# Performance work log

Measured on AMD Instinct MI355X. Metric: run time of the kernel, lower is better.

Reference implementation:

```python
import jax, jax.numpy as jnp
import numpy as np

B, N, FEAT, H, E, L = 4096, 64, 32, 128, 4, 3  # batch, node_num, node feat, hidden_dim, edge_dim, hidden_num


def setup_inputs() -> dict:
    key = jax.random.key(0)
    ks = jax.random.split(key, 12)
    s = 0.05
    x = jax.random.normal(ks[0], (B, N, FEAT), dtype=jnp.float32)
    adj = jax.random.uniform(ks[1], (B, E, N, N), dtype=jnp.float32)
    # per-node input/output embeddings (stacked over node index)
    in_w = jax.random.normal(ks[2], (N, FEAT, H), dtype=jnp.float32) * s
    in_b = jax.random.normal(ks[3], (N, H), dtype=jnp.float32) * s
    out_w = jax.random.normal(ks[4], (N, H, FEAT), dtype=jnp.float32) * s
    out_b = jax.random.normal(ks[5], (N, FEAT), dtype=jnp.float32) * s
    # relational GC weights per layer: (L, E, H, H) and bias (L, E, 1, H)
    gc_w = jax.random.normal(ks[6], (L, E, H, H), dtype=jnp.float32) * s
    gc_b = jax.random.normal(ks[7], (L, E, 1, H), dtype=jnp.float32) * s
    # GRU params, gate order [r, z, n] like torch
    w_ih = jax.random.normal(ks[8], (3 * H, H), dtype=jnp.float32) * s
    w_hh = jax.random.normal(ks[9], (3 * H, H), dtype=jnp.float32) * s
    b_ih = jax.random.normal(ks[10], (3 * H,), dtype=jnp.float32) * s
    b_hh = jax.random.normal(ks[11], (3 * H,), dtype=jnp.float32) * s
    return {"x": x, "adj": adj, "in_w": in_w, "in_b": in_b, "out_w": out_w,
            "out_b": out_b, "gc_w": gc_w, "gc_b": gc_b, "w_ih": w_ih,
            "w_hh": w_hh, "b_ih": b_ih, "b_hh": b_hh}


def _gru_step(xf, h, w_ih, w_hh, b_ih, b_hh):
    # xf, h: (B*N, H); single-timestep torch GRU cell
    gi = xf @ w_ih.T + b_ih
    gh = h @ w_hh.T + b_hh
    i_r, i_z, i_n = jnp.split(gi, 3, axis=-1)
    h_r, h_z, h_n = jnp.split(gh, 3, axis=-1)
    r = jax.nn.sigmoid(i_r + h_r)
    z = jax.nn.sigmoid(i_z + h_z)
    n = jnp.tanh(i_n + r * h_n)
    return (1.0 - z) * n + z * h


def reference(x, adj, in_w, in_b, out_w, out_b, gc_w, gc_b, w_ih, w_hh, b_ih, b_hh):
    # per-node input embedding: (B, N, FEAT) -> (B, N, H)
    h = jnp.einsum('bnd,ndh->bnh', x, in_w) + in_b
    hidden = h.reshape(-1, H)  # initial GRU hidden = embedded input
    cur = h
    for i in range(L):
        # relational GCN: per-edge-type projection + adjacency matmul + bias + relu + mean over edge types
        support = jnp.einsum('bid,edh->beih', cur, gc_w[i])
        out = jnp.einsum('beij,bejh->beih', adj, support) + gc_b[i]
        out = jax.nn.relu(out)
        agg = jnp.mean(out, axis=1)  # (B, N, H)
        hidden = _gru_step(agg.reshape(-1, H), hidden, w_ih, w_hh, b_ih, b_hh)
        cur = hidden.reshape(B, N, H)
    # per-node output embedding, zero-padded back to hidden width
    feats = jnp.einsum('bnh,nhd->bnd', cur, out_w) + out_b  # (B, N, FEAT)
    return jnp.pad(feats, ((0, 0), (0, 0), (0, H - FEAT)))
```

## Files before the change

### kernel.cpp

```cpp
#include <hip/hip_runtime.h>
#include <cstdint>

#define NBATCH 4096
#define NNODE  64
#define FEAT   32
#define H      128
#define NE     4
#define NL     3

typedef __attribute__((ext_vector_type(8))) short short8;
typedef __attribute__((ext_vector_type(4))) short short4v;
typedef __attribute__((ext_vector_type(4))) float f32x4;
typedef __attribute__((ext_vector_type(2))) float f32x2;
typedef unsigned long long u64;
typedef unsigned short ushort;

#define IMG_GC_ELEMS   (128 * 64)
#define IMG_GRU_ELEMS  (48 * 128)
#define IMG_GC_BYTES   (24 * IMG_GC_ELEMS * 2)
#define IMG_GRU_BYTES  (16 * IMG_GRU_ELEMS * 2)
#define WS_W_BYTES     (IMG_GC_BYTES + IMG_GRU_BYTES)
#define WIMG_SHORTS    (WS_W_BYTES / 2)
#define ADJ_IMG_ELEMS  4096
#define WS_FULL ((size_t)WS_W_BYTES + (size_t)NBATCH * NE * ADJ_IMG_ELEMS * 2)

__device__ __forceinline__ ushort f2b(float f) {
  union { float f; unsigned u; } v; v.f = f;
  unsigned u = v.u + 0x7FFFu + ((v.u >> 16) & 1u);
  return (ushort)(u >> 16);
}
__device__ __forceinline__ float b2f(ushort s) {
  union { unsigned u; float f; } v; v.u = ((unsigned)s) << 16;
  return v.f;
}
__device__ __forceinline__ unsigned cvtpk(float lo, float hi) {
  unsigned r;
  asm volatile("v_cvt_pk_bf16_f32 %0, %1, %2" : "=v"(r) : "v"(lo), "v"(hi));
  return r;
}
__device__ __forceinline__ u64 pk4(float a, float b, float c, float d) {
  return (u64)cvtpk(a, b) | ((u64)cvtpk(c, d) << 32);
}
__device__ __forceinline__ float sigm(float v) { return 1.0f / (1.0f + __expf(-v)); }
__device__ __forceinline__ float tanh_(float v) {
  v = fminf(fmaxf(v, -15.f), 15.f);
  float e = __expf(-2.f * v);
  return (1.f - e) / (1.f + e);
}
__device__ __forceinline__ int gidx128(int r, int g) { return r * 128 + ((g ^ (r & 7)) << 3); }
__device__ __forceinline__ int idx128(int r, int k) { return gidx128(r, k >> 3) + (k & 7); }
__device__ __forceinline__ int gidx64(int r, int g) { return r * 64 + (((g ^ (r & 7)) & 7) << 3); }

__device__ __forceinline__ short8 pack8f(const float* v) {
  union { unsigned u[4]; short8 s; } r;
  r.u[0] = cvtpk(v[0], v[1]); r.u[1] = cvtpk(v[2], v[3]);
  r.u[2] = cvtpk(v[4], v[5]); r.u[3] = cvtpk(v[6], v[7]);
  return r.s;
}

__device__ __forceinline__ void gll16(const void* g, void* l) {
  __builtin_amdgcn_global_load_lds(
      (const __attribute__((address_space(1))) unsigned int*)g,
      (__attribute__((address_space(3))) unsigned int*)l, 16, 0, 0);
}

#define STAGE(dst, src, NIT)                                             \
  do {                                                                   \
    _Pragma("unroll")                                                    \
    for (int it_ = 0; it_ < (NIT); ++it_) {                              \
      int off_ = (it_ * 4 + w) * 1024;                                   \
      gll16((const char*)(src) + off_ + lane * 16, (char*)(dst) + off_); \
    }                                                                    \
  } while (0)

#define BAR() do { asm volatile("s_waitcnt lgkmcnt(0)" ::: "memory"); \
                   __builtin_amdgcn_s_barrier(); } while (0)
#define VMW(N) do { asm volatile("s_waitcnt vmcnt(" #N ")" ::: "memory"); \
                    __builtin_amdgcn_sched_barrier(0); } while (0)
#define SB0() __builtin_amdgcn_sched_barrier(0)

__global__ __launch_bounds__(256, 2) void k_prep(
    const float* __restrict__ gc_w, const float* __restrict__ w_ih,
    const float* __restrict__ w_hh, ushort* __restrict__ ws)
{
  const int t = threadIdx.x;
  if (blockIdx.x < 24) {
    const int blk = blockIdx.x;
    const int kh = blk & 1, e = (blk >> 1) & 3, l = blk >> 3;
    const float* We = gc_w + (size_t)(l * NE + e) * H * H;
    ushort* dst = ws + (size_t)blk * IMG_GC_ELEMS;
    #pragma unroll
    for (int it = 0; it < 4; ++it) {
      int idx = t + it * 256;
      int r = idx >> 3, g = idx & 7;
      float v[8];
      #pragma unroll
      for (int j = 0; j < 8; ++j) v[j] = We[(kh * 64 + g * 8 + j) * H + r];
      *(short8*)&dst[gidx64(r, g)] = pack8f(v);
    }
  } else {
    const int blk = blockIdx.x - 24;
    const int c = blk & 7, m = blk >> 3;
    const float* Mat = m ? w_hh : w_ih;
    ushort* dst = ws + WIMG_SHORTS - IMG_GRU_BYTES / 2 + (size_t)blk * IMG_GRU_ELEMS;
    #pragma unroll
    for (int it = 0; it < 3; ++it) {
      int idx = t + it * 256;
      int rr = idx >> 4, g = idx & 15;
      int mrow = (rr >> 4) * H + 16 * c + (rr & 15);
      float v[8];
      #pragma unroll
      for (int j = 0; j < 8; ++j) v[j] = Mat[mrow * H + g * 8 + j];
      *(short8*)&dst[gidx128(rr, g)] = pack8f(v);
    }
  }
}

template <bool ADJIMG>
__global__ __launch_bounds__(256, 2) void k_inemb(
    const float* __restrict__ x, const float* __restrict__ in_w,
    const float* __restrict__ in_b, const float* __restrict__ adj,
    ushort* __restrict__ ws, float* __restrict__ out)
{
  __shared__ float s_wt[FEAT * H];
  __shared__ float s_x[64 * FEAT];
  const int t = threadIdx.x;
  const int n = blockIdx.x >> 6, bt = blockIdx.x & 63, b0 = bt * 64;
  const float* wsrc = in_w + (size_t)n * FEAT * H;
  #pragma unroll
  for (int it = 0; it < 4; ++it) {
    int i4 = t + it * 256;
    *(f32x4*)&s_wt[i4 * 4] = *(const f32x4*)&wsrc[i4 * 4];
  }
  {
    int r = t >> 2, q = t & 3;
    const float* xs = x + ((size_t)(b0 + r) * NNODE + n) * FEAT;
    *(f32x4*)&s_x[r * 32 + q * 8]     = *(const f32x4*)&xs[q * 8];
    *(f32x4*)&s_x[r * 32 + q * 8 + 4] = *(const f32x4*)&xs[q * 8 + 4];
  }
  __syncthreads();
  const int h2 = t & 63, rp = t >> 6;
  const float bi0 = in_b[n * H + 2 * h2], bi1 = in_b[n * H + 2 * h2 + 1];
  #pragma unroll 1
  for (int m = 0; m < 16; ++m) {
    int r = rp + 4 * m;
    float a0 = bi0, a1 = bi1;
    #pragma unroll
    for (int d = 0; d < 32; ++d) {
      float xv = s_x[r * 32 + d];
      f32x2 wv = *(const f32x2*)&s_wt[d * H + 2 * h2];
      a0 += xv * wv.x; a1 += xv * wv.y;
    }
    unsigned p = cvtpk(a0, a1);
    ushort* tail = (ushort*)(out + ((size_t)(b0 + r) * NNODE + n) * H + 64);
    *(unsigned*)(tail + 2 * h2) = p;
  }
  if (ADJIMG) {
    const float* ab = adj + (size_t)blockIdx.x * NE * NNODE * NNODE;
    ushort* dst = ws + WIMG_SHORTS + (size_t)blockIdx.x * NE * ADJ_IMG_ELEMS;
    #pragma unroll 1
    for (int q = 0; q < 8; ++q) {
      int gi = t + q * 256;
      int e = gi >> 9, idx = gi & 511, r = idx >> 3, g = idx & 7;
      const float* src = ab + e * 4096 + r * 64 + g * 8;
      float v[8];
      #pragma unroll
      for (int j = 0; j < 8; ++j) v[j] = src[j];
      *(short8*)&dst[e * ADJ_IMG_ELEMS + gidx64(r, g)] = pack8f(v);
    }
  }
}

template <bool ADJIMG>
__global__ __launch_bounds__(256, 2) void k_main(
    const float* __restrict__ adj,
    const float* __restrict__ gc_b,
    const float* __restrict__ b_ih, const float* __restrict__ b_hh,
    const ushort* __restrict__ wimg,
    float* __restrict__ out)
{
  __shared__ ushort s_u[128 * 64];
  __shared__ ushort s_stage[24576];
  __shared__ float s_bias[1280];

  ushort* w0    = s_stage;
  ushort* w1    = s_stage + 8192;
  ushort* sadj  = s_stage + 16384;
  ushort* gru0  = s_stage;
  ushort* gru1  = s_stage + 12288;

  const int t = threadIdx.x;
  const int b = blockIdx.x;
  const int w = t >> 6, lane = t & 63, lr = lane & 15, lq = lane >> 4;
  const int wm = w & 1, wn = w >> 1;
  float* outb = out + (size_t)b * NNODE * H;
  const ushort* img_gru = wimg + WIMG_SHORTS - IMG_GRU_BYTES / 2;
  const ushort* aimg = wimg + WIMG_SHORTS + (size_t)b * NE * ADJ_IMG_ELEMS;

  STAGE(w0, wimg, 4);
  short8 cur[2][4];
  #pragma unroll
  for (int rt = 0; rt < 2; ++rt)
    #pragma unroll
    for (int ks = 0; ks < 4; ++ks) {
      int node = 32 * wm + 16 * rt + lr;
      cur[rt][ks] = *(const short8*)((const ushort*)(outb + (size_t)node * H + 64) + 32 * ks + 8 * lq);
    }
  #pragma unroll
  for (int it = 0; it < 3; ++it) {
    int idx = t + it * 256;
    s_bias[512 + idx] = (idx < 384) ? b_ih[idx] : b_hh[idx - 384];
  }
  __syncthreads();

  #pragma unroll 1
  for (int layer = 0; layer < NL; ++layer) {
    f32x4 agg[2][4];
    #pragma unroll
    for (int mt = 0; mt < 2; ++mt)
      #pragma unroll
      for (int nt = 0; nt < 4; ++nt) agg[mt][nt] = f32x4{0.f, 0.f, 0.f, 0.f};

    #pragma unroll 1
    for (int e = 0; e < NE; ++e) {
      const ushort* img_e = wimg + (size_t)((layer * NE + e) * 2) * IMG_GC_ELEMS;

      if (e == 0) {
        s_bias[t]       = gc_b[layer * 512 + t];
        s_bias[t + 256] = gc_b[layer * 512 + t + 256];
      }
      STAGE(w1, img_e + IMG_GC_ELEMS, 4);
      SB0();
      if (ADJIMG) {
        STAGE(sadj, aimg + (size_t)e * ADJ_IMG_ELEMS, 2);
        SB0();
      } else {
        const float* adj_e = adj + (((size_t)b * NE + e) * NNODE * NNODE);
        #pragma unroll
        for (int it = 0; it < 2; ++it) {
          int idx = t + it * 256;
          int i = idx >> 3, g = idx & 7;
          const float* src = adj_e + i * 64 + g * 8;
          float v[8];
          #pragma unroll
          for (int j = 0; j < 8; ++j) v[j] = src[j];
          *(short8*)&sadj[gidx64(i, g)] = pack8f(v);
        }
      }
      f32x4 Sacc[2][4];
      #pragma unroll
      for (int mt = 0; mt < 2; ++mt)
        #pragma unroll
        for (int nt = 0; nt < 4; ++nt) Sacc[mt][nt] = f32x4{0.f, 0.f, 0.f, 0.f};
      if (ADJIMG) VMW(6);
      __builtin_amdgcn_s_setprio(1);
      #pragma unroll
      for (int ks = 0; ks < 2; ++ks) {
        #pragma unroll
        for (int nt = 0; nt < 4; ++nt) {
          short8 bb = *(const short8*)&w0[gidx64(64 * wn + 16 * nt + lr, ks * 4 + lq)];
          #pragma unroll
          for (int mt = 0; mt < 2; ++mt)
            Sacc[mt][nt] = __builtin_amdgcn_mfma_f32_16x16x32_bf16(cur[mt][ks], bb, Sacc[mt][nt], 0, 0, 0);
        }
      }
      __builtin_amdgcn_s_setprio(0);
      if (ADJIMG) { VMW(2); BAR(); } else __syncthreads();

      if (e < 3) { STAGE(w0, img_e + 2 * IMG_GC_ELEMS, 4); }
      else       { STAGE(gru0, img_gru, 3); }
      SB0();
      __builtin_amdgcn_s_setprio(1);
      #pragma unroll
      for (int ks = 0; ks < 2; ++ks) {
        #pragma unroll
        for (int nt = 0; nt < 4; ++nt) {
          short8 bb = *(const short8*)&w1[gidx64(64 * wn + 16 * nt + lr, ks * 4 + lq)];
          #pragma unroll
          for (int mt = 0; mt < 2; ++mt)
            Sacc[mt][nt] = __builtin_amdgcn_mfma_f32_16x16x32_bf16(cur[mt][2 + ks], bb, Sacc[mt][nt], 0, 0, 0);
        }
      }
      __builtin_amdgcn_s_setprio(0);
      #pragma unroll
      for (int mt = 0; mt < 2; ++mt) {
        int j0 = 32 * wm + 16 * mt + 4 * lq;
        #pragma unroll
        for (int nt = 0; nt < 4; ++nt) {
          int h = 64 * wn + 16 * nt + lr;
          *(u64*)&s_u[gidx64(h, j0 >> 3) + (j0 & 7)] =
              pk4(Sacc[mt][nt][0], Sacc[mt][nt][1], Sacc[mt][nt][2], Sacc[mt][nt][3]);
        }
      }
      if (ADJIMG) { if (e < 3) { VMW(4); } else { VMW(3); } BAR(); } else __syncthreads();

      if (e == 3) { STAGE(gru0 + 6144, img_gru + IMG_GRU_ELEMS, 3); SB0(); }
      {
        f32x4 Oacc[2][4];
        #pragma unroll
        for (int mt = 0; mt < 2; ++mt)
          #pragma unroll
          for (int nt = 0; nt < 4; ++nt) Oacc[mt][nt] = f32x4{0.f, 0.f, 0.f, 0.f};
        __builtin_amdgcn_s_setprio(1);
        #pragma unroll
        for (int ks = 0; ks < 2; ++ks) {
          short8 a[2];
          #pragma unroll
          for (int mt = 0; mt < 2; ++mt)
            a[mt] = *(const short8*)&sadj[gidx64(32 * wm + 16 * mt + lr, ks * 4 + lq)];
          #pragma unroll
          for (int nt = 0; nt < 4; ++nt) {
            short8 bb = *(const short8*)&s_u[gidx64(64 * wn + 16 * nt + lr, ks * 4 + lq)];
            #pragma unroll
            for (int mt = 0; mt < 2; ++mt)
              Oacc[mt][nt] = __builtin_amdgcn_mfma_f32_16x16x32_bf16(a[mt], bb, Oacc[mt][nt], 0, 0, 0);
          }
        }
        __builtin_amdgcn_s_setprio(0);
        #pragma unroll
        for (int mt = 0; mt < 2; ++mt)
          #pragma unroll
          for (int nt = 0; nt < 4; ++nt) {
            float bias = s_bias[e * 128 + 64 * wn + 16 * nt + lr];
            #pragma unroll
            for (int r = 0; r < 4; ++r)
              agg[mt][nt][r] += 0.25f * fmaxf(Oacc[mt][nt][r] + bias, 0.f);
          }
      }
      if (ADJIMG) { BAR(); } else __syncthreads();
    }

    #pragma unroll
    for (int mt = 0; mt < 2; ++mt)
      #pragma unroll
      for (int nt = 0; nt < 4; ++nt) {
        int h = 64 * wn + 16 * nt + lr;
        #pragma unroll
        for (int r = 0; r < 4; ++r)
          s_u[idx128(32 * wm + 16 * mt + 4 * lq + r, h)] = f2b(agg[mt][nt][r]);
      }
    __syncthreads();

    #pragma unroll 1
    for (int p = 0; p < 4; ++p) {
      const int cc = 2 * p + wn;
      const ushort* ihb = gru0 + wn * 6144;
      const ushort* hhb = gru1 + wn * 6144;
      STAGE(gru1, img_gru + (size_t)(8 + 2 * p) * IMG_GRU_ELEMS, 3);
      STAGE(gru1 + 6144, img_gru + (size_t)(8 + 2 * p + 1) * IMG_GRU_ELEMS, 3);
      SB0();
      short4v holdv[2];
      #pragma unroll
      for (int nst = 0; nst < 2; ++nst) {
        int node = 16 * (2 * wm + nst) + lr;
        holdv[nst] = *(const short4v*)((const ushort*)(outb + (size_t)node * H + 64) + 16 * cc + 4 * lq);
      }
      f32x4 gi[3][2];
      #pragma unroll
      for (int tg = 0; tg < 3; ++tg)
        #pragma unroll
        for (int nst = 0; nst < 2; ++nst) gi[tg][nst] = f32x4{0.f, 0.f, 0.f, 0.f};
      __builtin_amdgcn_s_setprio(1);
      #pragma unroll
      for (int ks = 0; ks < 4; ++ks) {
        short8 bb[2];
        #pragma unroll
        for (int nst = 0; nst < 2; ++nst)
          bb[nst] = *(const short8*)&s_u[gidx128(16 * (2 * wm + nst) + lr, ks * 4 + lq)];
        #pragma unroll
        for (int tg = 0; tg < 3; ++tg) {
          short8 a = *(const short8*)&ihb[gidx128(16 * tg + lr, ks * 4 + lq)];
          #pragma unroll
          for (int nst = 0; nst < 2; ++nst)
            gi[tg][nst] = __builtin_amdgcn_mfma_f32_16x16x32_bf16(a, bb[nst], gi[tg][nst], 0, 0, 0);
        }
      }
      __builtin_amdgcn_s_setprio(0);
      __syncthreads();

      if (p < 3) {
        STAGE(gru0, img_gru + (size_t)(2 * (p + 1)) * IMG_GRU_ELEMS, 3);
        STAGE(gru0 + 6144, img_gru + (size_t)(2 * (p + 1) + 1) * IMG_GRU_ELEMS, 3);
      } else if (layer < 2) {
        STAGE(w0, wimg + (size_t)((layer + 1) * NE * 2) * IMG_GC_ELEMS, 4);
      }
      SB0();
      f32x4 gh[3][2];
      #pragma unroll
      for (int tg = 0; tg < 3; ++tg)
        #pragma unroll
        for (int nst = 0; nst < 2; ++nst) gh[tg][nst] = f32x4{0.f, 0.f, 0.f, 0.f};
      __builtin_amdgcn_s_setprio(1);
      #pragma unroll
      for (int ks = 0; ks < 4; ++ks) {
        #pragma unroll
        for (int tg = 0; tg < 3; ++tg) {
          short8 a = *(const short8*)&hhb[gidx128(16 * tg + lr, ks * 4 + lq)];
          #pragma unroll
          for (int nst = 0; nst < 2; ++nst)
            gh[tg][nst] = __builtin_amdgcn_mfma_f32_16x16x32_bf16(a, cur[nst][ks], gh[tg][nst], 0, 0, 0);
        }
      }
      __builtin_amdgcn_s_setprio(0);
      #pragma unroll
      for (int nst = 0; nst < 2; ++nst) {
        int node = 16 * (2 * wm + nst) + lr;
        float hf[4];
        #pragma unroll
        for (int r = 0; r < 4; ++r) {
          int mH = 16 * cc + 4 * lq + r;
          float rg = sigm(gi[0][nst][r] + s_bias[512 + mH] + gh[0][nst][r] + s_bias[896 + mH]);
          float zg = sigm(gi[1][nst][r] + s_bias[640 + mH] + gh[1][nst][r] + s_bias[1024 + mH]);
          float ng = tanh_(gi[2][nst][r] + s_bias[768 + mH] + rg * (gh[2][nst][r] + s_bias[1152 + mH]));
          float hold = b2f((ushort)holdv[nst][r]);
          hf[r] = (1.f - zg) * ng + zg * hold;
        }
        *(u64*)((ushort*)(outb + (size_t)node * H + 64) + 16 * cc + 4 * lq) =
            pk4(hf[0], hf[1], hf[2], hf[3]);
      }
      __syncthreads();
    }

    if (layer < 2) {
      #pragma unroll
      for (int rt = 0; rt < 2; ++rt)
        #pragma unroll
        for (int ks = 0; ks < 4; ++ks) {
          int node = 32 * wm + 16 * rt + lr;
          cur[rt][ks] = *(const short8*)((const ushort*)(outb + (size_t)node * H + 64) + 32 * ks + 8 * lq);
        }
    }
  }
}

__global__ __launch_bounds__(256, 2) void k_outemb(
    const float* __restrict__ out_w, const float* __restrict__ out_b,
    float* __restrict__ out)
{
  __shared__ float s_wt[H * FEAT];
  __shared__ float s_c[64 * 132];
  const int t = threadIdx.x;
  const int n = blockIdx.x >> 6, bt = blockIdx.x & 63, b0 = bt * 64;
  const float* wsrc = out_w + (size_t)n * H * FEAT;
  #pragma unroll
  for (int it = 0; it < 4; ++it) {
    int i4 = t + it * 256;
    *(f32x4*)&s_wt[i4 * 4] = *(const f32x4*)&wsrc[i4 * 4];
  }
  #pragma unroll
  for (int it = 0; it < 4; ++it) {
    int idx = t + it * 256;
    int r = idx >> 4, g = idx & 15;
    const ushort* tail = (const ushort*)(out + ((size_t)(b0 + r) * NNODE + n) * H + 64);
    short8 v = *(const short8*)(tail + g * 8);
    #pragma unroll
    for (int j = 0; j < 8; ++j) s_c[r * 132 + g * 8 + j] = b2f((ushort)v[j]);
  }
  __syncthreads();
  const int d = t & 31, rq = t >> 5;
  const float bias = out_b[n * FEAT + d];
  float accs[8];
  #pragma unroll
  for (int m = 0; m < 8; ++m) {
    int r = rq + 8 * m;
    float a = bias;
    #pragma unroll 8
    for (int k = 0; k < H; ++k) a += s_c[r * 132 + k] * s_wt[k * FEAT + d];
    accs[m] = a;
  }
  #pragma unroll
  for (int m = 0; m < 8; ++m) {
    int r = rq + 8 * m;
    out[((size_t)(b0 + r) * NNODE + n) * H + d] = accs[m];
  }
  #pragma unroll
  for (int q = 0; q < 6; ++q) {
    int idx = t + q * 256;
    int r = idx / 24, c4 = idx - r * 24;
    *(f32x4*)&out[((size_t)(b0 + r) * NNODE + n) * H + FEAT + c4 * 4] =
        f32x4{0.f, 0.f, 0.f, 0.f};
  }
}

extern "C" void kernel_launch(void* const* d_in, const int* in_sizes, int n_in,
                              void* d_out, int out_size, void* d_ws, size_t ws_size,
                              hipStream_t stream) {
  const float* x     = (const float*)d_in[0];
  const float* adj   = (const float*)d_in[1];
  const float* in_w  = (const float*)d_in[2];
  const float* in_b  = (const float*)d_in[3];
  const float* out_w = (const float*)d_in[4];
  const float* out_b = (const float*)d_in[5];
  const float* gc_w  = (const float*)d_in[6];
  const float* gc_b  = (const float*)d_in[7];
  const float* w_ih  = (const float*)d_in[8];
  const float* w_hh  = (const float*)d_in[9];
  const float* b_ih  = (const float*)d_in[10];
  const float* b_hh  = (const float*)d_in[11];
  (void)in_sizes; (void)n_in; (void)out_size;
  ushort* wimg = (ushort*)d_ws;
  const bool full = ws_size >= WS_FULL;
  hipLaunchKernelGGL(k_prep, dim3(40), dim3(256), 0, stream, gc_w, w_ih, w_hh, wimg);
  if (full) {
    hipLaunchKernelGGL(k_inemb<true>, dim3(NBATCH), dim3(256), 0, stream,
                       x, in_w, in_b, adj, wimg, (float*)d_out);
    hipLaunchKernelGGL(k_main<true>, dim3(NBATCH), dim3(256), 0, stream,
                       adj, gc_b, b_ih, b_hh, wimg, (float*)d_out);
  } else {
    hipLaunchKernelGGL(k_inemb<false>, dim3(NBATCH), dim3(256), 0, stream,
                       x, in_w, in_b, adj, wimg, (float*)d_out);
    hipLaunchKernelGGL(k_main<false>, dim3(NBATCH), dim3(256), 0, stream,
                       adj, gc_b, b_ih, b_hh, wimg, (float*)d_out);
  }
  hipLaunchKernelGGL(k_outemb, dim3(NBATCH), dim3(256), 0, stream, out_w, out_b, (float*)d_out);
}
```

Baseline: 763.9 us.

## Read weight fragments directly from global memory instead of staging through LDS

Removes the double-buffered LDS staging (global_load_lds, waitcnt and sched barriers) for the GC and GRU weight images. The MFMA B/A fragments are now loaded straight from global memory and served by the L2/L1 caches. This shrinks shared memory enough to raise launch bounds to 4 blocks per CU and drops several barriers. In exchange, every wave issues redundant global loads with exposed latency and loses the explicit prefetch overlap.

```diff
diff --git a/kernel.cpp b/kernel.cpp
--- a/kernel.cpp
+++ b/kernel.cpp
@@ -73,11 +73,8 @@
     }                                                                    \
   } while (0)
 
-#define BAR() do { asm volatile("s_waitcnt lgkmcnt(0)" ::: "memory"); \
-                   __builtin_amdgcn_s_barrier(); } while (0)
-#define VMW(N) do { asm volatile("s_waitcnt vmcnt(" #N ")" ::: "memory"); \
-                    __builtin_amdgcn_sched_barrier(0); } while (0)
-#define SB0() __builtin_amdgcn_sched_barrier(0)
+#define MFMA16(A, B, C) __builtin_amdgcn_mfma_f32_16x16x32_bf16((A), (B), (C), 0, 0, 0)
+#define GFRAG(base, off) (*(const short8*)&(base)[(off)])
 
 __global__ __launch_bounds__(256, 2) void k_prep(
     const float* __restrict__ gc_w, const float* __restrict__ w_ih,
@@ -172,40 +169,30 @@
 }
 
 template <bool ADJIMG>
-__global__ __launch_bounds__(256, 2) void k_main(
+__global__ __launch_bounds__(256, 4) void k_main(
     const float* __restrict__ adj,
     const float* __restrict__ gc_b,
     const float* __restrict__ b_ih, const float* __restrict__ b_hh,
     const ushort* __restrict__ wimg,
     float* __restrict__ out)
 {
-  __shared__ ushort s_u[128 * 64];
-  __shared__ ushort s_stage[24576];
-  __shared__ float s_bias[1280];
-
-  ushort* w0    = s_stage;
-  ushort* w1    = s_stage + 8192;
-  ushort* sadj  = s_stage + 16384;
-  ushort* gru0  = s_stage;
-  ushort* gru1  = s_stage + 12288;
-
-  const int t = threadIdx.x;
-  const int b = blockIdx.x;
+  __shared__ ushort s_u[8192];
+  __shared__ ushort s_adj[4096];
+  __shared__ float  s_bias[1280];
+
+  const int t = threadIdx.x, b = blockIdx.x;
   const int w = t >> 6, lane = t & 63, lr = lane & 15, lq = lane >> 4;
   const int wm = w & 1, wn = w >> 1;
   float* outb = out + (size_t)b * NNODE * H;
   const ushort* img_gru = wimg + WIMG_SHORTS - IMG_GRU_BYTES / 2;
   const ushort* aimg = wimg + WIMG_SHORTS + (size_t)b * NE * ADJ_IMG_ELEMS;
 
-  STAGE(w0, wimg, 4);
   short8 cur[2][4];
   #pragma unroll
-  for (int rt = 0; rt < 2; ++rt)
-    #pragma unroll
-    for (int ks = 0; ks < 4; ++ks) {
-      int node = 32 * wm + 16 * rt + lr;
-      cur[rt][ks] = *(const short8*)((const ushort*)(outb + (size_t)node * H + 64) + 32 * ks + 8 * lq);
-    }
+  for (int mt = 0; mt < 2; ++mt)
+    #pragma unroll
+    for (int ks = 0; ks < 4; ++ks)
+      cur[mt][ks] = *(const short8*)((const ushort*)(outb + (size_t)(32 * wm + 16 * mt + lr) * H + 64) + 32 * ks + 8 * lq);
   #pragma unroll
   for (int it = 0; it < 3; ++it) {
     int idx = t + it * 256;
@@ -224,16 +211,12 @@
     #pragma unroll 1
     for (int e = 0; e < NE; ++e) {
       const ushort* img_e = wimg + (size_t)((layer * NE + e) * 2) * IMG_GC_ELEMS;
-
       if (e == 0) {
         s_bias[t]       = gc_b[layer * 512 + t];
         s_bias[t + 256] = gc_b[layer * 512 + t + 256];
       }
-      STAGE(w1, img_e + IMG_GC_ELEMS, 4);
-      SB0();
       if (ADJIMG) {
-        STAGE(sadj, aimg + (size_t)e * ADJ_IMG_ELEMS, 2);
-        SB0();
+        STAGE(s_adj, aimg + (size_t)e * ADJ_IMG_ELEMS, 2);
       } else {
         const float* adj_e = adj + (((size_t)b * NE + e) * NNODE * NNODE);
         #pragma unroll
@@ -244,7 +227,7 @@
           float v[8];
           #pragma unroll
           for (int j = 0; j < 8; ++j) v[j] = src[j];
-          *(short8*)&sadj[gidx64(i, g)] = pack8f(v);
+          *(short8*)&s_adj[gidx64(i, g)] = pack8f(v);
         }
       }
       f32x4 Sacc[2][4];
@@ -252,33 +235,19 @@
       for (int mt = 0; mt < 2; ++mt)
         #pragma unroll
         for (int nt = 0; nt < 4; ++nt) Sacc[mt][nt] = f32x4{0.f, 0.f, 0.f, 0.f};
-      if (ADJIMG) VMW(6);
       __builtin_amdgcn_s_setprio(1);
       #pragma unroll
-      for (int ks = 0; ks < 2; ++ks) {
-        #pragma unroll
-        for (int nt = 0; nt < 4; ++nt) {
-          short8 bb = *(const short8*)&w0[gidx64(64 * wn + 16 * nt + lr, ks * 4 + lq)];
-          #pragma unroll
-          for (int mt = 0; mt < 2; ++mt)
-            Sacc[mt][nt] = __builtin_amdgcn_mfma_f32_16x16x32_bf16(cur[mt][ks], bb, Sacc[mt][nt], 0, 0, 0);
-        }
-      }
-      __builtin_amdgcn_s_setprio(0);
-      if (ADJIMG) { VMW(2); BAR(); } else __syncthreads();
-
-      if (e < 3) { STAGE(w0, img_e + 2 * IMG_GC_ELEMS, 4); }
-      else       { STAGE(gru0, img_gru, 3); }
-      SB0();
-      __builtin_amdgcn_s_setprio(1);
-      #pragma unroll
-      for (int ks = 0; ks < 2; ++ks) {
-        #pragma unroll
-        for (int nt = 0; nt < 4; ++nt) {
-          short8 bb = *(const short8*)&w1[gidx64(64 * wn + 16 * nt + lr, ks * 4 + lq)];
-          #pragma unroll
-          for (int mt = 0; mt < 2; ++mt)
-            Sacc[mt][nt] = __builtin_amdgcn_mfma_f32_16x16x32_bf16(cur[mt][2 + ks], bb, Sacc[mt][nt], 0, 0, 0);
+      for (int kh = 0; kh < 2; ++kh) {
+        const ushort* wb = img_e + (size_t)kh * IMG_GC_ELEMS;
+        #pragma unroll
+        for (int ks = 0; ks < 2; ++ks) {
+          #pragma unroll
+          for (int nt = 0; nt < 4; ++nt) {
+            short8 bb = GFRAG(wb, gidx64(64 * wn + 16 * nt + lr, ks * 4 + lq));
+            #pragma unroll
+            for (int mt = 0; mt < 2; ++mt)
+              Sacc[mt][nt] = MFMA16(cur[mt][2 * kh + ks], bb, Sacc[mt][nt]);
+          }
         }
       }
       __builtin_amdgcn_s_setprio(0);
@@ -292,9 +261,8 @@
               pk4(Sacc[mt][nt][0], Sacc[mt][nt][1], Sacc[mt][nt][2], Sacc[mt][nt][3]);
         }
       }
-      if (ADJIMG) { if (e < 3) { VMW(4); } else { VMW(3); } BAR(); } else __syncthreads();
-
-      if (e == 3) { STAGE(gru0 + 6144, img_gru + IMG_GRU_ELEMS, 3); SB0(); }
+      __syncthreads();
+
       {
         f32x4 Oacc[2][4];
         #pragma unroll
@@ -307,13 +275,13 @@
           short8 a[2];
           #pragma unroll
           for (int mt = 0; mt < 2; ++mt)
-            a[mt] = *(const short8*)&sadj[gidx64(32 * wm + 16 * mt + lr, ks * 4 + lq)];
+            a[mt] = *(const short8*)&s_adj[gidx64(32 * wm + 16 * mt + lr, ks * 4 + lq)];
           #pragma unroll
           for (int nt = 0; nt < 4; ++nt) {
             short8 bb = *(const short8*)&s_u[gidx64(64 * wn + 16 * nt + lr, ks * 4 + lq)];
             #pragma unroll
             for (int mt = 0; mt < 2; ++mt)
-              Oacc[mt][nt] = __builtin_amdgcn_mfma_f32_16x16x32_bf16(a[mt], bb, Oacc[mt][nt], 0, 0, 0);
+              Oacc[mt][nt] = MFMA16(a[mt], bb, Oacc[mt][nt]);
           }
         }
         __builtin_amdgcn_s_setprio(0);
@@ -327,7 +295,7 @@
               agg[mt][nt][r] += 0.25f * fmaxf(Oacc[mt][nt][r] + bias, 0.f);
           }
       }
-      if (ADJIMG) { BAR(); } else __syncthreads();
+      __syncthreads();
     }
 
     #pragma unroll
@@ -344,22 +312,20 @@
     #pragma unroll 1
     for (int p = 0; p < 4; ++p) {
       const int cc = 2 * p + wn;
-      const ushort* ihb = gru0 + wn * 6144;
-      const ushort* hhb = gru1 + wn * 6144;
-      STAGE(gru1, img_gru + (size_t)(8 + 2 * p) * IMG_GRU_ELEMS, 3);
-      STAGE(gru1 + 6144, img_gru + (size_t)(8 + 2 * p + 1) * IMG_GRU_ELEMS, 3);
-      SB0();
+      const ushort* ihg = img_gru + (size_t)cc * IMG_GRU_ELEMS;
+      const ushort* hhg = img_gru + (size_t)(8 + cc) * IMG_GRU_ELEMS;
       short4v holdv[2];
       #pragma unroll
-      for (int nst = 0; nst < 2; ++nst) {
-        int node = 16 * (2 * wm + nst) + lr;
-        holdv[nst] = *(const short4v*)((const ushort*)(outb + (size_t)node * H + 64) + 16 * cc + 4 * lq);
-      }
-      f32x4 gi[3][2];
+      for (int nst = 0; nst < 2; ++nst)
+        holdv[nst] = *(const short4v*)((const ushort*)(outb + (size_t)(16 * (2 * wm + nst) + lr) * H + 64) + 16 * cc + 4 * lq);
+      f32x4 gi[3][2], gh[3][2];
       #pragma unroll
       for (int tg = 0; tg < 3; ++tg)
         #pragma unroll
-        for (int nst = 0; nst < 2; ++nst) gi[tg][nst] = f32x4{0.f, 0.f, 0.f, 0.f};
+        for (int nst = 0; nst < 2; ++nst) {
+          gi[tg][nst] = f32x4{0.f, 0.f, 0.f, 0.f};
+          gh[tg][nst] = f32x4{0.f, 0.f, 0.f, 0.f};
+        }
       __builtin_amdgcn_s_setprio(1);
       #pragma unroll
       for (int ks = 0; ks < 4; ++ks) {
@@ -369,36 +335,20 @@
           bb[nst] = *(const short8*)&s_u[gidx128(16 * (2 * wm + nst) + lr, ks * 4 + lq)];
         #pragma unroll
         for (int tg = 0; tg < 3; ++tg) {
-          short8 a = *(const short8*)&ihb[gidx128(16 * tg + lr, ks * 4 + lq)];
+          short8 a = GFRAG(ihg, gidx128(16 * tg + lr, ks * 4 + lq));
           #pragma unroll
           for (int nst = 0; nst < 2; ++nst)
-            gi[tg][nst] = __builtin_amdgcn_mfma_f32_16x16x32_bf16(a, bb[nst], gi[tg][nst], 0, 0, 0);
-        }
-      }
-      __builtin_amdgcn_s_setprio(0);
-      __syncthreads();
-
-      if (p < 3) {
-        STAGE(gru0, img_gru + (size_t)(2 * (p + 1)) * IMG_GRU_ELEMS, 3);
-        STAGE(gru0 + 6144, img_gru + (size_t)(2 * (p + 1) + 1) * IMG_GRU_ELEMS, 3);
-      } else if (layer < 2) {
-        STAGE(w0, wimg + (size_t)((layer + 1) * NE * 2) * IMG_GC_ELEMS, 4);
-      }
-      SB0();
-      f32x4 gh[3][2];
-      #pragma unroll
-      for (int tg = 0; tg < 3; ++tg)
-        #pragma unroll
-        for (int nst = 0; nst < 2; ++nst) gh[tg][nst] = f32x4{0.f, 0.f, 0.f, 0.f};
-      __builtin_amdgcn_s_setprio(1);
+            gi[tg][nst] = MFMA16(a, bb[nst], gi[tg][nst]);
+        }
+      }
       #pragma unroll
       for (int ks = 0; ks < 4; ++ks) {
         #pragma unroll
         for (int tg = 0; tg < 3; ++tg) {
-          short8 a = *(const short8*)&hhb[gidx128(16 * tg + lr, ks * 4 + lq)];
+          short8 a = GFRAG(hhg, gidx128(16 * tg + lr, ks * 4 + lq));
           #pragma unroll
           for (int nst = 0; nst < 2; ++nst)
-            gh[tg][nst] = __builtin_amdgcn_mfma_f32_16x16x32_bf16(a, cur[nst][ks], gh[tg][nst], 0, 0, 0);
+            gh[tg][nst] = MFMA16(a, cur[nst][ks], gh[tg][nst]);
         }
       }
       __builtin_amdgcn_s_setprio(0);
@@ -412,23 +362,20 @@
           float rg = sigm(gi[0][nst][r] + s_bias[512 + mH] + gh[0][nst][r] + s_bias[896 + mH]);
           float zg = sigm(gi[1][nst][r] + s_bias[640 + mH] + gh[1][nst][r] + s_bias[1024 + mH]);
           float ng = tanh_(gi[2][nst][r] + s_bias[768 + mH] + rg * (gh[2][nst][r] + s_bias[1152 + mH]));
-          float hold = b2f((ushort)holdv[nst][r]);
-          hf[r] = (1.f - zg) * ng + zg * hold;
+          hf[r] = (1.f - zg) * ng + zg * b2f((ushort)holdv[nst][r]);
         }
         *(u64*)((ushort*)(outb + (size_t)node * H + 64) + 16 * cc + 4 * lq) =
             pk4(hf[0], hf[1], hf[2], hf[3]);
       }
-      __syncthreads();
-    }
+    }
+    __syncthreads();
 
     if (layer < 2) {
       #pragma unroll
-      for (int rt = 0; rt < 2; ++rt)
-        #pragma unroll
-        for (int ks = 0; ks < 4; ++ks) {
-          int node = 32 * wm + 16 * rt + lr;
-          cur[rt][ks] = *(const short8*)((const ushort*)(outb + (size_t)node * H + 64) + 32 * ks + 8 * lq);
-        }
+      for (int mt = 0; mt < 2; ++mt)
+        #pragma unroll
+        for (int ks = 0; ks < 4; ++ks)
+          cur[mt][ks] = *(const short8*)((const ushort*)(outb + (size_t)(32 * wm + 16 * mt + lr) * H + 64) + 32 * ks + 8 * lq);
     }
   }
 }
```

New measurement: 1.348 ms. +76.4%, slower.
